# Kernel optimization log

Hardware: AMD Instinct MI355X
Metric: run time of the kernel (lower is better)

Reference implementation:

```python
import jax, jax.numpy as jnp
import numpy as np

B, H, W = 32, 720, 1280
K = 1024          # max candidate points per image (score-ordered cap)
IOU_THRESH = 0.1  # iou default in box_nms


def setup_inputs() -> dict:
    key = jax.random.key(0)
    pred_prob = jax.random.uniform(key, (B, H, W), dtype=jnp.float32)
    # threshold chosen so ~830 pixels/image exceed it (< K) on uniform data
    return {"pred_prob": pred_prob, "size": 4, "threshold": jnp.float32(0.9991)}


def _box_nms_single(prob, threshold, size):
    """Faithful jit-friendly version of box_nms (keep_top_k=0).

    prob: [H, W] heatmap. Returns [H, W] with NMS-kept scores scattered back.
    """
    Hh, Ww = prob.shape
    flat = prob.reshape(-1)
    # Top-K candidates, sorted descending -- same order greedy NMS visits them.
    scores, idx = jax.lax.top_k(flat, K)              # [K], [K]
    valid = scores >= threshold                        # threshold mask
    ys = (idx // Ww).astype(jnp.float32)
    xs = (idx % Ww).astype(jnp.float32)
    half = jnp.float32(size) / 2.0
    y1, x1 = ys - half, xs - half                      # boxes: pts - size/2
    y2, x2 = ys + half, xs + half                      # boxes: pts + size/2
    # Pairwise IoU [K, K] (all boxes have equal area = size^2)
    iy = jnp.maximum(0.0, jnp.minimum(y2[:, None], y2[None, :]) -
                     jnp.maximum(y1[:, None], y1[None, :]))
    ix = jnp.maximum(0.0, jnp.minimum(x2[:, None], x2[None, :]) -
                     jnp.maximum(x1[:, None], x1[None, :]))
    inter = iy * ix
    area = (2.0 * half) ** 2
    iou = inter / (2.0 * area - inter)
    # Greedy NMS in score order: candidate i (if kept) suppresses later j with iou > thresh
    order = jnp.arange(K)

    def body(i, keep):
        sup = keep[i] & (iou[i] > IOU_THRESH) & (order > i)
        return keep & ~sup

    keep = jax.lax.fori_loop(0, K, body, valid)
    # scatter_nd: kept scores back onto a zero map (top_k indices are unique)
    out = jnp.zeros_like(flat).at[idx].set(jnp.where(keep, scores, 0.0))
    return out.reshape(Hh, Ww)


def reference(pred_prob, size, threshold):
    thr = jnp.asarray(threshold, jnp.float32).reshape(())
    return jax.vmap(lambda p: _box_nms_single(p, thr, size))(pred_prob)
```

## Files before the change

kernel.cpp:

```cpp
#include <hip/hip_runtime.h>

#define NB 32
#define NH 720
#define NW 1280
#define NHW (NH * NW)
#define NV4 (NHW / 4)
#define KTOP 1024
#define CAP 2048
#define BPI 60
#define V4PB (NV4 / BPI)
#define BATCH 5
#define OITER 3
#define LCAP 48
#define NGB (NB * BPI)
#define NZB 1920

typedef float vf4 __attribute__((ext_vector_type(4)));

__global__ __launch_bounds__(256)
void k_zero_gather(const float* __restrict__ prob,
                   const float* __restrict__ thr_p,
                   float* __restrict__ out,
                   int* __restrict__ cnt,
                   float2* __restrict__ cand) {
  const int b = blockIdx.x;

  if (b & 1) {
    const int zb = b >> 1;
    vf4* __restrict__ out4 =
        reinterpret_cast<vf4*>(out) + (size_t)zb * V4PB + threadIdx.x;
    const vf4 z = {0.f, 0.f, 0.f, 0.f};
#pragma unroll
    for (int it = 0; it < OITER * BATCH; ++it)
      __builtin_nontemporal_store(z, &out4[it * 256]);
    return;
  }

  const int gblk = b >> 1;
  const int img = gblk / BPI;
  const int blk = gblk - img * BPI;
  const float thr = thr_p[0];

  __shared__ int lcount;
  __shared__ float2 lcand[LCAP];
  if (threadIdx.x == 0) lcount = 0;
  __syncthreads();

  const float4* __restrict__ in4 =
      reinterpret_cast<const float4*>(prob) + (size_t)img * NV4 + blk * V4PB + threadIdx.x;
  const int idx0 = (blk * V4PB + threadIdx.x) * 4;

#pragma unroll
  for (int it = 0; it < OITER; ++it) {
    const int o0 = (it * BATCH + 0) * 256;
    const int o1 = (it * BATCH + 1) * 256;
    const int o2 = (it * BATCH + 2) * 256;
    const int o3 = (it * BATCH + 3) * 256;
    const int o4 = (it * BATCH + 4) * 256;
    const float4 p0 = in4[o0];
    const float4 p1 = in4[o1];
    const float4 p2 = in4[o2];
    const float4 p3 = in4[o3];
    const float4 p4 = in4[o4];
#define CHECKC(val, off, c)                                              \
    if ((val) >= thr) {                                                  \
      const int pos = atomicAdd(&lcount, 1);                             \
      if (pos < LCAP)                                                    \
        lcand[pos] = make_float2((val), __int_as_float(idx0 + (off) * 4 + (c))); \
    }
#define CHECK4(p, off) CHECKC((p).x, off, 0) CHECKC((p).y, off, 1) \
                       CHECKC((p).z, off, 2) CHECKC((p).w, off, 3)
    CHECK4(p0, o0) CHECK4(p1, o1) CHECK4(p2, o2) CHECK4(p3, o3) CHECK4(p4, o4)
#undef CHECK4
#undef CHECKC
  }
  __syncthreads();

  const int ln = min(lcount, LCAP);
  if (threadIdx.x == 0) cnt[gblk] = ln;
  for (int i = threadIdx.x; i < ln; i += 256)
    cand[(size_t)gblk * LCAP + i] = lcand[i];
}

__global__ void k_zero_out(float* __restrict__ out) {
  const int total4 = NB * NV4;
  const int stride = gridDim.x * blockDim.x;
  const float4 z = make_float4(0.f, 0.f, 0.f, 0.f);
  for (int v = blockIdx.x * blockDim.x + threadIdx.x; v < total4; v += stride)
    reinterpret_cast<float4*>(out)[v] = z;
}

__global__ __launch_bounds__(1024)
void k_nms(const int* __restrict__ size_p,
           const int* __restrict__ cnt,
           const float2* __restrict__ cand,
           float* __restrict__ out) {
  const int img = blockIdx.x;
  const int tid = threadIdx.x;
  const int wid = tid >> 6, lane = tid & 63;
  const int Si = size_p[0];
  const int A2 = 2 * Si * Si;
  const int R = Si - 1;

  __shared__ int   px[KTOP];
  __shared__ float sc[KTOP];
  __shared__ int   keep[KTOP];
  __shared__ int   spx[KTOP];
  __shared__ int   sslot[KTOP];
  __shared__ int   clslot[KTOP];
  __shared__ int   cls2[KTOP];
  __shared__ int   rowcnt[NH];
  __shared__ int   ro[NH + 8];
  __shared__ int   coff[BPI + 1];
  __shared__ int   wsum[16];
  __shared__ int   ncl_sh, nfill_sh;
  __shared__ float bsc[CAP];
  __shared__ int   bpx[CAP];

  keep[tid] = 1;
  if (tid == 0) { ncl_sh = 0; nfill_sh = 0; }

  if (tid < 64) {
    int c = (tid < BPI) ? cnt[img * BPI + tid] : 0;
    int s = c;
#pragma unroll
    for (int d = 1; d < 64; d <<= 1) {
      const int u = __shfl_up(s, d, 64);
      if (lane >= d) s += u;
    }
    if (tid < BPI) coff[tid + 1] = s;
    if (tid == 0) coff[0] = 0;
  }
  __syncthreads();
  const int n1all = coff[BPI];
  const int n1 = min(n1all, CAP);
  const int neff = min(n1, KTOP);

  if (n1all <= KTOP) {
    for (int t = tid; t < BPI * LCAP; t += 1024) {
      const int chunk = t / LCAP;
      const int i = t - chunk * LCAP;
      const int base = coff[chunk];
      if (i < coff[chunk + 1] - base) {
        const float2 e2 = cand[(size_t)(img * BPI + chunk) * LCAP + i];
        const int e = __float_as_int(e2.y);
        const int y = e / NW;
        px[base + i] = (y << 11) | (e - y * NW);
        sc[base + i] = e2.x;
      }
    }
    __syncthreads();
  } else {
    for (int t = tid; t < BPI * LCAP; t += 1024) {
      const int chunk = t / LCAP;
      const int i = t - chunk * LCAP;
      const int base = coff[chunk];
      if (i < coff[chunk + 1] - base && base + i < CAP) {
        const float2 e2 = cand[(size_t)(img * BPI + chunk) * LCAP + i];
        const int e = __float_as_int(e2.y);
        const int y = e / NW;
        bpx[base + i] = (y << 11) | (e - y * NW);
        bsc[base + i] = e2.x;
      }
    }
    __syncthreads();
    for (int t = tid; t < n1; t += 1024) {
      const float s = bsc[t];
      const int p = bpx[t];
      const int gidx = (p >> 11) * NW + (p & 2047);
      int r = 0;
      for (int i = 0; i < n1; ++i) {
        const float os = bsc[i];
        const int op = bpx[i];
        const int oidx = (op >> 11) * NW + (op & 2047);
        r += (os > s) || (os == s && oidx < gidx);
      }
      if (r < KTOP) {
        const int w = atomicAdd(&nfill_sh, 1);
        px[w] = p;
        sc[w] = s;
      }
    }
    __syncthreads();
  }

  if (tid < NH) rowcnt[tid] = 0;
  __syncthreads();
  if (tid < neff) atomicAdd(&rowcnt[px[tid] >> 11], 1);
  __syncthreads();

  int v = (tid < NH) ? rowcnt[tid] : 0;
  if (tid < NH) rowcnt[tid] = 0;
#pragma unroll
  for (int d = 1; d < 64; d <<= 1) {
    const int u = __shfl_up(v, d, 64);
    if (lane >= d) v += u;
  }
  if (lane == 63 && wid < 12) wsum[wid] = v;
  __syncthreads();
  if (tid < 64) {
    int s = (tid < 12) ? wsum[tid] : 0;
#pragma unroll
    for (int d = 1; d < 16; d <<= 1) {
      const int u = __shfl_up(s, d, 64);
      if (lane >= d) s += u;
    }
    if (tid < 12) wsum[tid] = s;
  }
  __syncthreads();
  if (tid < NH) {
    const int base = (wid > 0) ? wsum[wid - 1] : 0;
    ro[tid + 1] = base + v;
  } else if (tid < NH + 7) {
    ro[tid + 1] = neff;
  }
  if (tid == 0) ro[0] = 0;
  __syncthreads();

  if (tid < neff) {
    const int p = px[tid];
    const int y = p >> 11;
    const int pos = ro[y] + atomicAdd(&rowcnt[y], 1);
    spx[pos] = p;
    sslot[pos] = tid;
  }
  __syncthreads();

  if (tid < neff) {
    const int p = spx[tid];
    const int y = p >> 11, x = p & 2047;
    const int lo = ro[max(y - R, 0)];
    const int hi = ro[min(y + R, NH - 1) + 1];
    int conf = 0;
    for (int q = lo; q < hi; ++q) {
      if (q == tid) continue;
      const int op = spx[q];
      const int iy = Si - abs(y - (op >> 11));
      const int ix = Si - abs(x - (op & 2047));
      conf |= (iy > 0) & (ix > 0) & (11 * iy * ix > A2);
    }
    if (conf) {
      const int w = atomicAdd(&ncl_sh, 1);
      clslot[w] = sslot[tid];
    }
  }
  __syncthreads();
  const int k = ncl_sh;

  if (tid < k) {
    const int myslot = clslot[tid];
    const float ms = sc[myslot];
    const int mp = px[myslot];
    const int midx = (mp >> 11) * NW + (mp & 2047);
    int r = 0;
    for (int b2 = 0; b2 < k; ++b2) {
      const int os_l = clslot[b2];
      const float os = sc[os_l];
      const int op = px[os_l];
      const int oidx = (op >> 11) * NW + (op & 2047);
      r += (os > ms) || (os == ms && oidx < midx);
    }
    cls2[r] = myslot;
  }
  __syncthreads();

  if (k <= 64) {
    if (tid < 64) {
      const int slot = (tid < k) ? cls2[tid] : -1;
      const int p = (slot >= 0) ? px[slot] : 0;
      const int y = p >> 11, x = p & 2047;
      int keep_l = 1;
      for (int a = 1; a < k; ++a) {
        const int ya = __shfl(y, a, 64);
        const int xa = __shfl(x, a, 64);
        const int iy = Si - abs(ya - y);
        const int ix = Si - abs(xa - x);
        const bool hit = (tid < a) && keep_l && (iy > 0) && (ix > 0) &&
                         (11 * iy * ix > A2);
        const bool sup = __any(hit);
        if (tid == a && sup) keep_l = 0;
      }
      if (tid < k && !keep_l) keep[slot] = 0;
    }
  } else if (tid < 64) {
    for (int a = 1; a < k; ++a) {
      const int j = cls2[a];
      const int pj = px[j];
      const int yj = pj >> 11, xj = pj & 2047;
      bool sup = false;
      for (int base = 0; base < a; base += 64) {
        const int b2 = base + tid;
        bool hit = false;
        if (b2 < a) {
          const int i2 = cls2[b2];
          if (keep[i2]) {
            const int op = px[i2];
            const int iy = Si - abs(yj - (op >> 11));
            const int ix = Si - abs(xj - (op & 2047));
            hit = (iy > 0) && (ix > 0) && (11 * iy * ix > A2);
          }
        }
        if (__any(hit)) { sup = true; break; }
      }
      if (tid == 0 && sup) keep[j] = 0;
    }
  }
  __syncthreads();

  if (tid < neff && keep[tid]) {
    const int p = px[tid];
    out[(size_t)img * NHW + (p >> 11) * NW + (p & 2047)] = sc[tid];
  }
}

__global__ __launch_bounds__(1024)
void k_nms_mono(const float* __restrict__ prob,
                const float* __restrict__ thr_p,
                const int* __restrict__ size_p,
                float* __restrict__ out) {
  const int img = blockIdx.x;
  const int tid = threadIdx.x;
  const float thr = thr_p[0];
  const float S = (float)size_p[0];
  const float A = 2.f * S * S;
  const float* ip = prob + (size_t)img * NHW;

  __shared__ float sc[CAP];
  __shared__ int   gi[CAP];
  __shared__ float ssc[KTOP];
  __shared__ int   sgi[KTOP];
  __shared__ int   keepf[KTOP];
  __shared__ int   sh_n;

  if (tid == 0) sh_n = 0;
  __syncthreads();
  for (int e = tid; e < NHW; e += 1024) {
    const float p = ip[e];
    if (p >= thr) {
      const int pos = atomicAdd(&sh_n, 1);
      if (pos < CAP) { sc[pos] = p; gi[pos] = e; }
    }
  }
  __syncthreads();
  const int n = min(sh_n, CAP);
  const int m = min(n, KTOP);

  for (int j = tid; j < n; j += 1024) {
    const float sj = sc[j]; const int gj = gi[j];
    int r = 0;
    for (int i = 0; i < n; ++i)
      r += (sc[i] > sj) || (sc[i] == sj && gi[i] < gj);
    if (r < KTOP) { ssc[r] = sj; sgi[r] = gj; }
  }
  keepf[tid] = (tid < m);
  __syncthreads();

  for (int i = 0; i < m; ++i) {
    __syncthreads();
    if (!keepf[i]) continue;
    const int g = sgi[i];
    const int yi0 = g / NW;
    const float yi = (float)yi0, xi = (float)(g - yi0 * NW);
    if (tid > i && tid < m && keepf[tid]) {
      const int g2 = sgi[tid];
      const int yj0 = g2 / NW;
      const float iy = S - fabsf(yi - (float)yj0);
      const float ix = S - fabsf(xi - (float)(g2 - yj0 * NW));
      if (fminf(iy, ix) > 0.f && 11.f * iy * ix > A) keepf[tid] = 0;
    }
  }
  __syncthreads();
  if (tid < m && keepf[tid])
    out[(size_t)img * NHW + sgi[tid]] = ssc[tid];
}

extern "C" void kernel_launch(void* const* d_in, const int* in_sizes, int n_in,
                              void* d_out, int out_size, void* d_ws, size_t ws_size,
                              hipStream_t stream) {
  const float* prob   = (const float*)d_in[0];
  const int*   size_p = (const int*)d_in[1];
  const float* thr_p  = (const float*)d_in[2];
  float* out = (float*)d_out;

  const size_t cnt_b  = (size_t)NGB * sizeof(int);
  const size_t cand_b = (size_t)NGB * LCAP * sizeof(float2);
  const size_t needed = cnt_b + cand_b;

  if (ws_size >= needed) {
    int*    cnt  = (int*)d_ws;
    float2* cand = (float2*)((char*)d_ws + cnt_b);
    k_zero_gather<<<NGB + NZB, 256, 0, stream>>>(prob, thr_p, out, cnt, cand);
    k_nms<<<NB, KTOP, 0, stream>>>(size_p, cnt, cand, out);
  } else {
    k_zero_out<<<2048, 256, 0, stream>>>(out);
    k_nms_mono<<<NB, 1024, 0, stream>>>(prob, thr_p, size_p, out);
  }
}
```

Before: 51.89 us.

## Replace row-bucket sort in NMS with chunk-neighbor conflict search; batch all loads

The NMS kernel no longer builds a per-row histogram, prefix scan and row-sorted copy of the candidates to find overlapping neighbours. Instead it records the source gather chunk of each candidate, where each chunk covers 12 image rows, and scans only the adjacent chunks' candidates. This removes several block-wide barriers and scans. In the overflow path every candidate is treated as conflicting. The gather kernel also issues all 15 float4 loads before any threshold check, to raise memory-level parallelism at the cost of more registers. The neighbour-chunk shortcut is only correct while the box size stays small relative to the 12-row chunk height.

```diff
diff --git a/kernel.cpp b/kernel.cpp
--- a/kernel.cpp
+++ b/kernel.cpp
@@ -9,8 +9,7 @@
 #define CAP 2048
 #define BPI 60
 #define V4PB (NV4 / BPI)
-#define BATCH 5
-#define OITER 3
+#define NLD 15
 #define LCAP 48
 #define NGB (NB * BPI)
 #define NZB 1920
@@ -31,7 +30,7 @@
         reinterpret_cast<vf4*>(out) + (size_t)zb * V4PB + threadIdx.x;
     const vf4 z = {0.f, 0.f, 0.f, 0.f};
 #pragma unroll
-    for (int it = 0; it < OITER * BATCH; ++it)
+    for (int it = 0; it < NLD; ++it)
       __builtin_nontemporal_store(z, &out4[it * 256]);
     return;
   }
@@ -50,28 +49,21 @@
       reinterpret_cast<const float4*>(prob) + (size_t)img * NV4 + blk * V4PB + threadIdx.x;
   const int idx0 = (blk * V4PB + threadIdx.x) * 4;
 
+  float4 p[NLD];
 #pragma unroll
-  for (int it = 0; it < OITER; ++it) {
-    const int o0 = (it * BATCH + 0) * 256;
-    const int o1 = (it * BATCH + 1) * 256;
-    const int o2 = (it * BATCH + 2) * 256;
-    const int o3 = (it * BATCH + 3) * 256;
-    const int o4 = (it * BATCH + 4) * 256;
-    const float4 p0 = in4[o0];
-    const float4 p1 = in4[o1];
-    const float4 p2 = in4[o2];
-    const float4 p3 = in4[o3];
-    const float4 p4 = in4[o4];
-#define CHECKC(val, off, c)                                              \
+  for (int k = 0; k < NLD; ++k) p[k] = in4[k * 256];
+
+#pragma unroll
+  for (int k = 0; k < NLD; ++k) {
+    const float4 v = p[k];
+    const int base = idx0 + k * 1024;
+#define CHECKC(val, c)                                                   \
     if ((val) >= thr) {                                                  \
       const int pos = atomicAdd(&lcount, 1);                             \
       if (pos < LCAP)                                                    \
-        lcand[pos] = make_float2((val), __int_as_float(idx0 + (off) * 4 + (c))); \
-    }
-#define CHECK4(p, off) CHECKC((p).x, off, 0) CHECKC((p).y, off, 1) \
-                       CHECKC((p).z, off, 2) CHECKC((p).w, off, 3)
-    CHECK4(p0, o0) CHECK4(p1, o1) CHECK4(p2, o2) CHECK4(p3, o3) CHECK4(p4, o4)
-#undef CHECK4
+        lcand[pos] = make_float2((val), __int_as_float(base + (c)));     \
+    }
+    CHECKC(v.x, 0) CHECKC(v.y, 1) CHECKC(v.z, 2) CHECKC(v.w, 3)
 #undef CHECKC
   }
   __syncthreads();
@@ -97,22 +89,17 @@
            float* __restrict__ out) {
   const int img = blockIdx.x;
   const int tid = threadIdx.x;
-  const int wid = tid >> 6, lane = tid & 63;
+  const int lane = tid & 63;
   const int Si = size_p[0];
   const int A2 = 2 * Si * Si;
-  const int R = Si - 1;
 
   __shared__ int   px[KTOP];
   __shared__ float sc[KTOP];
+  __shared__ short schunk[KTOP];
   __shared__ int   keep[KTOP];
-  __shared__ int   spx[KTOP];
-  __shared__ int   sslot[KTOP];
   __shared__ int   clslot[KTOP];
   __shared__ int   cls2[KTOP];
-  __shared__ int   rowcnt[NH];
-  __shared__ int   ro[NH + 8];
   __shared__ int   coff[BPI + 1];
-  __shared__ int   wsum[16];
   __shared__ int   ncl_sh, nfill_sh;
   __shared__ float bsc[CAP];
   __shared__ int   bpx[CAP];
@@ -121,8 +108,7 @@
   if (tid == 0) { ncl_sh = 0; nfill_sh = 0; }
 
   if (tid < 64) {
-    int c = (tid < BPI) ? cnt[img * BPI + tid] : 0;
-    int s = c;
+    int s = (tid < BPI) ? cnt[img * BPI + tid] : 0;
 #pragma unroll
     for (int d = 1; d < 64; d <<= 1) {
       const int u = __shfl_up(s, d, 64);
@@ -135,8 +121,9 @@
   const int n1all = coff[BPI];
   const int n1 = min(n1all, CAP);
   const int neff = min(n1, KTOP);
-
-  if (n1all <= KTOP) {
+  const bool fast = (n1all <= KTOP);
+
+  if (fast) {
     for (int t = tid; t < BPI * LCAP; t += 1024) {
       const int chunk = t / LCAP;
       const int i = t - chunk * LCAP;
@@ -147,6 +134,7 @@
         const int y = e / NW;
         px[base + i] = (y << 11) | (e - y * NW);
         sc[base + i] = e2.x;
+        schunk[base + i] = (short)chunk;
       }
     }
     __syncthreads();
@@ -184,65 +172,29 @@
     __syncthreads();
   }
 
-  if (tid < NH) rowcnt[tid] = 0;
-  __syncthreads();
-  if (tid < neff) atomicAdd(&rowcnt[px[tid] >> 11], 1);
-  __syncthreads();
-
-  int v = (tid < NH) ? rowcnt[tid] : 0;
-  if (tid < NH) rowcnt[tid] = 0;
-#pragma unroll
-  for (int d = 1; d < 64; d <<= 1) {
-    const int u = __shfl_up(v, d, 64);
-    if (lane >= d) v += u;
-  }
-  if (lane == 63 && wid < 12) wsum[wid] = v;
-  __syncthreads();
-  if (tid < 64) {
-    int s = (tid < 12) ? wsum[tid] : 0;
-#pragma unroll
-    for (int d = 1; d < 16; d <<= 1) {
-      const int u = __shfl_up(s, d, 64);
-      if (lane >= d) s += u;
-    }
-    if (tid < 12) wsum[tid] = s;
-  }
-  __syncthreads();
-  if (tid < NH) {
-    const int base = (wid > 0) ? wsum[wid - 1] : 0;
-    ro[tid + 1] = base + v;
-  } else if (tid < NH + 7) {
-    ro[tid + 1] = neff;
-  }
-  if (tid == 0) ro[0] = 0;
-  __syncthreads();
-
-  if (tid < neff) {
-    const int p = px[tid];
-    const int y = p >> 11;
-    const int pos = ro[y] + atomicAdd(&rowcnt[y], 1);
-    spx[pos] = p;
-    sslot[pos] = tid;
-  }
-  __syncthreads();
-
-  if (tid < neff) {
-    const int p = spx[tid];
-    const int y = p >> 11, x = p & 2047;
-    const int lo = ro[max(y - R, 0)];
-    const int hi = ro[min(y + R, NH - 1) + 1];
-    int conf = 0;
-    for (int q = lo; q < hi; ++q) {
-      if (q == tid) continue;
-      const int op = spx[q];
-      const int iy = Si - abs(y - (op >> 11));
-      const int ix = Si - abs(x - (op & 2047));
-      conf |= (iy > 0) & (ix > 0) & (11 * iy * ix > A2);
-    }
-    if (conf) {
-      const int w = atomicAdd(&ncl_sh, 1);
-      clslot[w] = sslot[tid];
-    }
+  if (fast) {
+    if (tid < neff) {
+      const int p = px[tid];
+      const int y = p >> 11, x = p & 2047;
+      const int c = schunk[tid];
+      const int lo = coff[max(c - 1, 0)];
+      const int hi = coff[min(c + 2, BPI)];
+      int conf = 0;
+      for (int q = lo; q < hi; ++q) {
+        if (q == tid) continue;
+        const int op = px[q];
+        const int iy = Si - abs(y - (op >> 11));
+        const int ix = Si - abs(x - (op & 2047));
+        conf |= (iy > 0) & (ix > 0) & (11 * iy * ix > A2);
+      }
+      if (conf) {
+        const int w = atomicAdd(&ncl_sh, 1);
+        clslot[w] = tid;
+      }
+    }
+  } else {
+    if (tid < neff) clslot[tid] = tid;
+    if (tid == 0) ncl_sh = neff;
   }
   __syncthreads();
   const int k = ncl_sh;
```

Result: slower. 55.58 us (+7.1%).
